# Performance work log

Hardware: AMD Instinct MI355X
Metric: run time of the kernel (lower is better)

## Reference

```python
import jax, jax.numpy as jnp
import numpy as np

B, C, H, W = 8, 128, 64, 64
D_STATE = 16
D_CONV = 4
EXPAND = 1.25
D_INNER = int(EXPAND * C)        # 160
DT_RANK = int(np.ceil(C / 16))   # 8


def setup_inputs() -> dict:
    key = jax.random.key(0)
    ks = jax.random.split(key, 10)
    f = lambda k, s, sc=0.02: jax.random.normal(k, s, dtype=jnp.float32) * sc
    return {
        "x": jax.random.normal(ks[0], (B, C, H, W), dtype=jnp.float32),
        "ln_g": jnp.ones((C,), jnp.float32),
        "ln_b": jnp.zeros((C,), jnp.float32),
        "in_proj_w": f(ks[1], (2 * D_INNER, C)),
        "conv_w": f(ks[2], (D_INNER, 1, D_CONV)),            # depthwise causal conv kernel
        "conv_b": jnp.zeros((D_INNER,), jnp.float32),
        "x_proj_w": f(ks[3], (DT_RANK + 2 * D_STATE, D_INNER)),
        "dt_proj_w": f(ks[4], (D_INNER, DT_RANK), 0.1),
        "dt_proj_b": f(ks[5], (D_INNER,), 0.1),
        # S4-style init: A_log = log(1..d_state) per inner channel (frozen in torch module)
        "A_log": jnp.log(jnp.tile(jnp.arange(1, D_STATE + 1, dtype=jnp.float32), (D_INNER, 1))),
        "D_param": jnp.ones((D_INNER,), jnp.float32),
        "out_proj_w": f(ks[6], (C, D_INNER)),
        "fuse_w": f(ks[7], (C, 2 * C)),                      # 1x1 conv == per-token matmul
        "scale": jnp.ones((1,), jnp.float32) * 0.1,
    }


def _layernorm(x, g, b, eps=1e-5):
    m = x.mean(-1, keepdims=True)
    v = x.var(-1, keepdims=True)
    return (x - m) * jax.lax.rsqrt(v + eps) * g + b


def _mamba(seq, in_proj_w, conv_w, conv_b, x_proj_w, dt_proj_w, dt_proj_b,
           A_log, D_param, out_proj_w):
    # seq: (B, L, C)
    Bsz, L, _ = seq.shape
    xz = jnp.einsum('blc,ec->ble', seq, in_proj_w)           # (B, L, 2*d_inner)
    xm, z = jnp.split(xz, 2, axis=-1)
    # depthwise causal conv over L, truncated to L (padding = d_conv-1 on the left)
    xc = jax.lax.conv_general_dilated(
        xm.transpose(0, 2, 1), conv_w, (1,), [(D_CONV - 1, 0)],
        feature_group_count=D_INNER, dimension_numbers=('NCH', 'OIH', 'NCH'))
    xm = jax.nn.silu((xc + conv_b[None, :, None]).transpose(0, 2, 1))  # (B, L, d_inner)
    x_dbl = jnp.einsum('bld,ed->ble', xm, x_proj_w)
    dt = x_dbl[..., :DT_RANK]
    Bm = x_dbl[..., DT_RANK:DT_RANK + D_STATE]               # (B, L, d_state)
    Cm = x_dbl[..., DT_RANK + D_STATE:]                      # (B, L, d_state)
    dt = jax.nn.softplus(jnp.einsum('blr,dr->bld', dt, dt_proj_w) + dt_proj_b)
    A = -jnp.exp(A_log)                                      # (d_inner, d_state)

    def step(h, inp):
        dt_t, B_t, C_t, x_t = inp                            # (B,d) (B,n) (B,n) (B,d)
        dA = jnp.exp(dt_t[:, :, None] * A)                   # (B, d_inner, d_state)
        h = dA * h + (dt_t * x_t)[:, :, None] * B_t[:, None, :]
        y = jnp.einsum('bdn,bn->bd', h, C_t)
        return h, y

    h0 = jnp.zeros((Bsz, D_INNER, D_STATE), dtype=seq.dtype)
    xs = (dt.transpose(1, 0, 2), Bm.transpose(1, 0, 2),
          Cm.transpose(1, 0, 2), xm.transpose(1, 0, 2))
    _, ys = jax.lax.scan(step, h0, xs)                       # ys: (L, B, d_inner)
    y = ys.transpose(1, 0, 2) + xm * D_param
    y = y * jax.nn.silu(z)
    return jnp.einsum('bld,cd->blc', y, out_proj_w)          # (B, L, C)


def reference(x, ln_g, ln_b, in_proj_w, conv_w, conv_b, x_proj_w, dt_proj_w,
              dt_proj_b, A_log, D_param, out_proj_w, fuse_w, scale):
    Bsz, Ch, Hh, Ww = x.shape
    seq = x.reshape(Bsz, Ch, Hh * Ww).transpose(0, 2, 1)     # (B, L, C) raster order
    seq_n = _layernorm(seq, ln_g, ln_b)                      # LN is per-token: commutes with flip
    args = (in_proj_w, conv_w, conv_b, x_proj_w, dt_proj_w, dt_proj_b,
            A_log, D_param, out_proj_w)
    y0 = _mamba(seq_n, *args)                                # forward raster scan
    y1 = _mamba(seq_n[:, ::-1, :], *args)[:, ::-1, :]        # reversed raster scan
    fused = jnp.einsum('blk,ck->blc', jnp.concatenate([y0, y1], axis=-1), fuse_w)
    out = seq + scale * fused                                # residual + learned scale
    return out.transpose(0, 2, 1).reshape(Bsz, Ch, Hh, Ww)
```

## Files before the change

### kernel.cpp

```cpp
#include <hip/hip_runtime.h>
#include <math.h>

#define LSEQ   4096
#define BATCH  8
#define CDIM   128
#define DIN    160
#define DSTATE 16
#define DTRANK 8
#define BLROWS (BATCH*LSEQ)
#define NCHUNK 128
#define TCH    32
#define SUBC   8
#define NSEG   16

typedef __attribute__((ext_vector_type(8))) short short8;
typedef __attribute__((ext_vector_type(8))) __bf16 bf16x8;
typedef __attribute__((ext_vector_type(4))) float float4v;
typedef __attribute__((ext_vector_type(2))) float f32x2;
typedef __attribute__((ext_vector_type(2))) unsigned u32x2;

__device__ __forceinline__ float4v mfma_bf16(short8 a, short8 b, float4v c) {
  return __builtin_amdgcn_mfma_f32_16x16x32_bf16(
      __builtin_bit_cast(bf16x8, a), __builtin_bit_cast(bf16x8, b), c, 0, 0, 0);
}

__device__ __forceinline__ unsigned short f2bf(float f) {
  union { float f; unsigned u; } v; v.f = f;
  unsigned r = v.u + 0x7FFF + ((v.u >> 16) & 1);
  return (unsigned short)(r >> 16);
}
__device__ __forceinline__ float bf2f(unsigned short h) {
  union { unsigned u; float f; } v; v.u = ((unsigned)h) << 16;
  return v.f;
}
__device__ __forceinline__ float f16tof(unsigned short h) {
  return (float)__builtin_bit_cast(_Float16, h);
}
__device__ __forceinline__ unsigned short ftof16(float f) {
  return __builtin_bit_cast(unsigned short, (_Float16)f);
}
__device__ __forceinline__ f32x2 pkfma(f32x2 a, f32x2 b, f32x2 c) {
#if __has_builtin(__builtin_elementwise_fma)
  return __builtin_elementwise_fma(a, b, c);
#else
  return a * b + c;
#endif
}
#define LO2(v) __builtin_shufflevector(v, v, 0, 1)
#define HI2(v) __builtin_shufflevector(v, v, 2, 3)

__global__ void prep_weights(const float* __restrict__ inpw, const float* __restrict__ xpw,
                             const float* __restrict__ fuse_w, const float* __restrict__ out_proj_w,
                             unsigned short* __restrict__ inpw_bf, unsigned short* __restrict__ xpw_bf,
                             unsigned short* __restrict__ W01) {
  int i = blockIdx.x * 256 + threadIdx.x;
  if (i < 320 * 128) inpw_bf[i] = f2bf(inpw[i]);
  if (i < 40 * 160)  xpw_bf[i]  = f2bf(xpw[i]);
  if (i < CDIM * DIN) {
    int d = i % DIN, c = i / DIN;
    float a0 = 0.f, a1 = 0.f;
    for (int k = 0; k < CDIM; ++k) {
      float o = out_proj_w[k * DIN + d];
      a0 += fuse_w[c * 256 + k] * o;
      a1 += fuse_w[c * 256 + 128 + k] * o;
    }
    W01[c * DIN + d] = f2bf(a0);
    W01[CDIM * DIN + c * DIN + d] = f2bf(a1);
  }
}

__global__ void ln_transpose_kernel(const float* __restrict__ x,
                                    const float* __restrict__ g,
                                    const float* __restrict__ bb,
                                    unsigned short* __restrict__ seqn) {
  __shared__ float sA[128 * 65];
  __shared__ float psum[2 * 256];
  __shared__ float mrs[2 * 64];
  int l0 = blockIdx.x * 64;
  int b  = blockIdx.y;
  int t  = threadIdx.x;
  int lsub = t & 63, crow = t >> 6;
  const float* xb = x + (size_t)b * CDIM * LSEQ;
  for (int it = 0; it < 32; ++it) {
    int c = crow + it * 4;
    sA[c * 65 + lsub] = xb[(size_t)c * LSEQ + l0 + lsub];
  }
  __syncthreads();
  float s = 0.f, ss = 0.f;
  for (int j = 0; j < 32; ++j) {
    int c = crow * 32 + j;
    float v = sA[c * 65 + lsub];
    s += v; ss += v * v;
  }
  psum[crow * 64 + lsub] = s;
  psum[256 + crow * 64 + lsub] = ss;
  __syncthreads();
  if (t < 64) {
    float su = 0.f, sq = 0.f;
    for (int p = 0; p < 4; ++p) { su += psum[p * 64 + t]; sq += psum[256 + p * 64 + t]; }
    float m = su * (1.f / 128.f);
    float var = sq * (1.f / 128.f) - m * m;
    mrs[t] = m;
    mrs[64 + t] = rsqrtf(var + 1e-5f);
  }
  __syncthreads();
  int c = t & 127, half = t >> 7;
  float gc = g[c], bc = bb[c];
  for (int it = 0; it < 32; ++it) {
    int l = it * 2 + half;
    float v = (sA[c * 65 + l] - mrs[l]) * mrs[64 + l] * gc + bc;
    seqn[((size_t)(b * LSEQ + l0 + l)) * CDIM + c] = f2bf(v);
  }
}

template<int K, bool MASKN, bool BF16OUT>
__global__ __launch_bounds__(256)
void gemm_mfma(const unsigned short* __restrict__ A0, const unsigned short* __restrict__ A1,
               const unsigned short* __restrict__ W,
               void* __restrict__ C0, void* __restrict__ C1, int N) {
  constexpr int LSTR = K + 8;
  __shared__ __align__(16) unsigned short As[64 * LSTR];
  __shared__ __align__(16) unsigned short Ws[64 * LSTR];
  const unsigned short* A = blockIdx.z ? A1 : A0;
  void* Cp = blockIdx.z ? C1 : C0;
  int m0 = blockIdx.x * 64;
  int n0 = blockIdx.y * 64;
  int t = threadIdx.x;
  constexpr int CH = 64 * K / 8;
  for (int c = t; c < CH; c += 256) {
    int row = c / (K / 8);
    int col = (c % (K / 8)) * 8;
    *(short8*)&As[row * LSTR + col] = *(const short8*)&A[(size_t)(m0 + row) * K + col];
    short8 wv = {};
    int nr = n0 + row;
    if (!MASKN || nr < N) wv = *(const short8*)&W[(size_t)nr * K + col];
    *(short8*)&Ws[row * LSTR + col] = wv;
  }
  __syncthreads();
  int lane = t & 63;
  int w = t >> 6;
  int l15 = lane & 15, quad = lane >> 4;
  float4v acc[4] = {};
#pragma unroll
  for (int kk = 0; kk < K; kk += 32) {
    short8 bfrag = *(const short8*)&Ws[(w * 16 + l15) * LSTR + kk + quad * 8];
#pragma unroll
    for (int i = 0; i < 4; ++i) {
      short8 afrag = *(const short8*)&As[(i * 16 + l15) * LSTR + kk + quad * 8];
      acc[i] = mfma_bf16(afrag, bfrag, acc[i]);
    }
  }
  int col = n0 + w * 16 + l15;
  if (MASKN && col >= N) return;
#pragma unroll
  for (int i = 0; i < 4; ++i)
#pragma unroll
    for (int r = 0; r < 4; ++r) {
      int row = m0 + i * 16 + quad * 4 + r;
      if (BF16OUT) ((unsigned short*)Cp)[(size_t)row * N + col] = f2bf(acc[i][r]);
      else         ((float*)Cp)[(size_t)row * N + col] = acc[i][r];
    }
}

__global__ void conv_silu_kernel(const unsigned short* __restrict__ xz,
                                 const float* __restrict__ cw,
                                 const float* __restrict__ cb,
                                 unsigned short* __restrict__ xm0,
                                 unsigned short* __restrict__ xm1,
                                 _Float16* __restrict__ szp) {
  int idx = blockIdx.x * 256 + threadIdx.x;
  int dir = blockIdx.y;
  if (idx >= BLROWS * 80) return;
  int dp = idx % 80;
  int bl = idx / 80;
  int l = bl % LSEQ, b = bl / LSEQ;
  int d = dp * 2;
  float w0[4], w1[4];
#pragma unroll
  for (int k = 0; k < 4; ++k) { w0[k] = cw[d * 4 + k]; w1[k] = cw[d * 4 + 4 + k]; }
  float a0 = cb[d], a1 = cb[d + 1];
  const unsigned short* base = xz + ((size_t)b * LSEQ) * 320 + d;
  if (dir == 0) {
#pragma unroll
    for (int k = 0; k < 4; ++k) {
      int lp = l - 3 + k;
      if (lp >= 0) {
        unsigned v = *(const unsigned*)&base[(size_t)lp * 320];
        a0 += w0[k] * bf2f((unsigned short)v);
        a1 += w1[k] * bf2f((unsigned short)(v >> 16));
      }
    }
  } else {
#pragma unroll
    for (int k = 0; k < 4; ++k) {
      int lp = l + 3 - k;
      if (lp < LSEQ) {
        unsigned v = *(const unsigned*)&base[(size_t)lp * 320];
        a0 += w0[k] * bf2f((unsigned short)v);
        a1 += w1[k] * bf2f((unsigned short)(v >> 16));
      }
    }
  }
  float s0 = a0 * __builtin_amdgcn_rcpf(1.f + __expf(-a0));
  float s1 = a1 * __builtin_amdgcn_rcpf(1.f + __expf(-a1));
  unsigned outv = (unsigned)f2bf(s0) | ((unsigned)f2bf(s1) << 16);
  unsigned short* xm = dir ? xm1 : xm0;
  *(unsigned*)&xm[(size_t)bl * DIN + d] = outv;
  if (dir == 0) {
    unsigned zv = *(const unsigned*)&xz[(size_t)bl * 320 + 160 + d];
    float z0 = bf2f((unsigned short)zv), z1 = bf2f((unsigned short)(zv >> 16));
    float g0 = z0 * __builtin_amdgcn_rcpf(1.f + __expf(-z0));
    float g1 = z1 * __builtin_amdgcn_rcpf(1.f + __expf(-z1));
    *(unsigned*)&szp[(size_t)bl * DIN + d] = (unsigned)ftof16(g0) | ((unsigned)ftof16(g1) << 16);
  }
}

__global__ void dtprep(const float* __restrict__ xdbl0, const float* __restrict__ xdbl1,
                       const float* __restrict__ dtw, const float* __restrict__ dtb,
                       unsigned* __restrict__ UR0, unsigned* __restrict__ UR1) {
  int idx = blockIdx.x * 256 + threadIdx.x;
  int dir = blockIdx.y;
  if (idx >= BLROWS * 80) return;
  int dp = idx % 80;
  int bl = idx / 80;
  const float* xdbl = dir ? xdbl1 : xdbl0;
  unsigned* UR = dir ? UR1 : UR0;
  float xr[8];
#pragma unroll
  for (int r = 0; r < 8; ++r) xr[r] = xdbl[(size_t)bl * 40 + r];
  unsigned out[2];
#pragma unroll
  for (int q = 0; q < 2; ++q) {
    int d = dp * 2 + q;
    float zz = dtb[d];
#pragma unroll
    for (int r = 0; r < 8; ++r) zz += xr[r] * dtw[d * 8 + r];
    float e  = __expf(fminf(zz, 20.f));
    float dt = (zz > 20.f) ? zz : __logf(1.f + e);
    float r1 = __builtin_amdgcn_rcpf(1.f + e);
    out[q] = (unsigned)ftof16(dt) | ((unsigned)ftof16(r1) << 16);
  }
  u32x2 o2 = { out[0], out[1] };
  *(u32x2*)&UR[(size_t)bl * DIN + dp * 2] = o2;
}

__global__ __launch_bounds__(320)
void scan_passA(const float* __restrict__ xdbl0, const float* __restrict__ xdbl1,
                const unsigned* __restrict__ UR0, const unsigned* __restrict__ UR1,
                const unsigned short* __restrict__ xm0v, const unsigned short* __restrict__ xm1v,
                const float* __restrict__ Dp,
                float* __restrict__ Q, float* __restrict__ rcf,
                unsigned* __restrict__ yr0, unsigned* __restrict__ yr1) {
  __shared__ __align__(16) float sBC[TCH * 32];
  int chunk = blockIdx.x, b = blockIdx.y, dir = blockIdx.z;
  int t = threadIdx.x;
  const float* xdbl = dir ? xdbl1 : xdbl0;
  const unsigned* UR = dir ? UR1 : UR0;
  const unsigned short* xm = dir ? xm1v : xm0v;
  unsigned* yr = dir ? yr1 : yr0;
  int l00 = dir ? (LSEQ - 1 - chunk * TCH) : (chunk * TCH);
  int step = dir ? -1 : 1;
  int rowbase = b * LSEQ + l00;
  for (int i = t; i < TCH * 32; i += 320) {
    int tt = i >> 5, j = i & 31;
    sBC[i] = xdbl[(size_t)(rowbase + step * tt) * 40 + 8 + j];
  }
  __syncthreads();
  int d = t >> 1, half = t & 1;
  float Dd = Dp[d];
  f32x2 h2[4] = {};
  float rcum = 1.f;
  const unsigned* urp = UR + (size_t)rowbase * DIN + d;
  const unsigned short* xmp = xm + (size_t)rowbase * DIN + d;
  unsigned* yrp = yr + (size_t)rowbase * DIN + d;
  int sstep = step * DIN;
  unsigned urb[4]; unsigned short xmb[4];
#pragma unroll
  for (int j = 0; j < 4; ++j) { urb[j] = urp[sstep * j]; xmb[j] = xmp[sstep * j]; }
  for (int g = 0; g < TCH / 4; ++g) {
#pragma unroll
    for (int j = 0; j < 4; ++j) {
      int tt = g * 4 + j;
      unsigned urv = urb[j];
      float xmv = bf2f(xmb[j]);
      if (g < TCH / 4 - 1) {
        urb[j] = urp[sstep * (tt + 4)];
        xmb[j] = xmp[sstep * (tt + 4)];
      }
      float dtv = f16tof((unsigned short)(urv & 0xFFFF));
      float r1  = f16tof((unsigned short)(urv >> 16));
      float u = dtv * xmv;
      rcum *= r1;
      float r2 = r1 * r1, r4 = r2 * r2, r8 = r4 * r4;
      float bs = half ? r8 : 1.f;
      f32x2 r2v = { r2, r2 };
      f32x2 p0 = { r1, r2 };
      f32x2 p1 = p0 * r2v;
      f32x2 p2 = p1 * r2v;
      f32x2 p3 = p2 * r2v;
      f32x2 bsv = { bs, bs };
      p0 *= bsv; p1 *= bsv; p2 *= bsv; p3 *= bsv;
      const float* bp = &sBC[tt * 32 + half * 8];
      float4v B0 = *(const float4v*)bp;
      float4v B1 = *(const float4v*)(bp + 4);
      float4v C0 = *(const float4v*)(bp + 16);
      float4v C1 = *(const float4v*)(bp + 20);
      f32x2 uv = { u, u };
      h2[0] = pkfma(p0, h2[0], uv * LO2(B0));
      h2[1] = pkfma(p1, h2[1], uv * HI2(B0));
      h2[2] = pkfma(p2, h2[2], uv * LO2(B1));
      h2[3] = pkfma(p3, h2[3], uv * HI2(B1));
      f32x2 ya = h2[0] * LO2(C0);
      ya = pkfma(h2[1], HI2(C0), ya);
      f32x2 yb = h2[2] * LO2(C1);
      yb = pkfma(h2[3], HI2(C1), yb);
      ya += yb;
      float ysc = ya[0] + ya[1];
      float yo = ysc + __shfl_xor(ysc, 1);
      if (half == 0) {
        float y = yo + Dd * xmv;
        yrp[sstep * tt] = (unsigned)f2bf(y) | ((unsigned)ftof16(rcum) << 16);
      }
    }
  }
  size_t base = (size_t)((dir * BATCH + b) * NCHUNK + chunk);
  float4v* qp = (float4v*)&Q[base * (DIN * 16) + d * 16 + half * 8];
  float4v q0 = { h2[0][0], h2[0][1], h2[1][0], h2[1][1] };
  float4v q1 = { h2[2][0], h2[2][1], h2[3][0], h2[3][1] };
  qp[0] = q0; qp[1] = q1;
  if (half == 0) rcf[base * DIN + d] = rcum;
}

__global__ __launch_bounds__(256)
void scan_passB(const float* Q, const float* __restrict__ rcf,
                float* Hinit) {
  __shared__ float sA[NSEG * 16], sQ[NSEG * 16];
  int blk = blockIdx.x;
  int d = blk % DIN;
  int rem = blk / DIN;
  int t = threadIdx.x;
  int n = t & 15, cs = t >> 4;
  unsigned k = n + 1;
  float a[SUBC], q[SUBC];
  float Aseg = 1.f, Qseg = 0.f;
#pragma unroll
  for (int j = 0; j < SUBC; ++j) {
    int ch = cs * SUBC + j;
    size_t base = (size_t)rem * NCHUNK + ch;
    float rf = rcf[base * DIN + d];
    float r2 = rf * rf, r4 = r2 * r2, r8 = r4 * r4;
    float av = 1.f;
    if (k & 1) av *= rf;
    if (k & 2) av *= r2;
    if (k & 4) av *= r4;
    if (k & 8) av *= r8;
    if (k & 16) av = r8 * r8;
    float qv = Q[base * (DIN * 16) + d * 16 + n];
    a[j] = av; q[j] = qv;
    Qseg = av * Qseg + qv;
    Aseg *= av;
  }
  sA[cs * 16 + n] = Aseg;
  sQ[cs * 16 + n] = Qseg;
  __syncthreads();
  if (t < 16) {
    float h = 0.f;
    for (int s = 0; s < NSEG; ++s) {
      float Av = sA[s * 16 + t], Qv = sQ[s * 16 + t];
      sA[s * 16 + t] = h;
      h = Av * h + Qv;
    }
  }
  __syncthreads();
  float h = sA[cs * 16 + n];
#pragma unroll
  for (int j = 0; j < SUBC; ++j) {
    int ch = cs * SUBC + j;
    size_t base = (size_t)rem * NCHUNK + ch;
    Hinit[base * (DIN * 16) + d * 16 + n] = h;
    h = a[j] * h + q[j];
  }
}

__global__ __launch_bounds__(192)
void scan_passC(const float* __restrict__ xdbl0, const float* __restrict__ xdbl1,
                const _Float16* __restrict__ szp,
                const float* __restrict__ Hinit,
                const unsigned* __restrict__ yr0, const unsigned* __restrict__ yr1,
                unsigned short* __restrict__ yg0, unsigned short* __restrict__ yg1) {
  __shared__ __align__(16) float sC[TCH * 16];
  int chunk = blockIdx.x, b = blockIdx.y, dir = blockIdx.z;
  int t = threadIdx.x;
  const float* xdbl = dir ? xdbl1 : xdbl0;
  const unsigned* yrb0 = dir ? yr1 : yr0;
  unsigned short* yg = dir ? yg1 : yg0;
  int l00 = dir ? (LSEQ - 1 - chunk * TCH) : (chunk * TCH);
  int step = dir ? -1 : 1;
  int rowbase = b * LSEQ + l00;
  for (int i = t; i < TCH * 16; i += 192)
    sC[i] = xdbl[(size_t)(rowbase + step * (i >> 4)) * 40 + 24 + (i & 15)];
  __syncthreads();
  if (t >= DIN) return;
  int d = t;
  size_t base = (size_t)((dir * BATCH + b) * NCHUNK + chunk);
  float4v H0v[4];
  const float4v* hp = (const float4v*)&Hinit[base * (DIN * 16) + d * 16];
#pragma unroll
  for (int n = 0; n < 4; ++n) H0v[n] = hp[n];
  const unsigned* yrp = yrb0 + (size_t)rowbase * DIN + d;
  const unsigned short* szq = (const unsigned short*)szp + (size_t)rowbase * DIN + d;
  unsigned short* ygp = yg + (size_t)rowbase * DIN + d;
  int sstep = step * DIN;
  unsigned yb[8]; unsigned short sb[8];
#pragma unroll
  for (int j = 0; j < 8; ++j) { yb[j] = yrp[sstep * j]; sb[j] = szq[sstep * j]; }
  for (int g = 0; g < TCH / 8; ++g) {
#pragma unroll
    for (int j = 0; j < 8; ++j) {
      int tt = g * 8 + j;
      unsigned v = yb[j];
      float sz = f16tof(sb[j]);
      if (g < TCH / 8 - 1) {
        yb[j] = yrp[sstep * (tt + 8)];
        sb[j] = szq[sstep * (tt + 8)];
      }
      float y = bf2f((unsigned short)v);
      float r1 = f16tof((unsigned short)(v >> 16));
      const float* cr = &sC[tt * 16];
      float4v Cv0 = *(const float4v*)cr;
      float4v Cv1 = *(const float4v*)(cr + 4);
      float4v Cv2 = *(const float4v*)(cr + 8);
      float4v Cv3 = *(const float4v*)(cr + 12);
      float r2 = r1 * r1;
      f32x2 r2v = { r2, r2 };
      f32x2 p0 = { r1, r2 };
      f32x2 p1 = p0 * r2v;
      f32x2 p2 = p1 * r2v;
      f32x2 p3 = p2 * r2v;
      f32x2 p4 = p3 * r2v;
      f32x2 p5 = p4 * r2v;
      f32x2 p6 = p5 * r2v;
      f32x2 p7 = p6 * r2v;
      f32x2 ca = p0 * (LO2(Cv0) * LO2(H0v[0]));
      ca = pkfma(p1, HI2(Cv0) * HI2(H0v[0]), ca);
      ca = pkfma(p2, LO2(Cv1) * LO2(H0v[1]), ca);
      ca = pkfma(p3, HI2(Cv1) * HI2(H0v[1]), ca);
      f32x2 cb2 = p4 * (LO2(Cv2) * LO2(H0v[2]));
      cb2 = pkfma(p5, HI2(Cv2) * HI2(H0v[2]), cb2);
      cb2 = pkfma(p6, LO2(Cv3) * LO2(H0v[3]), cb2);
      cb2 = pkfma(p7, HI2(Cv3) * HI2(H0v[3]), cb2);
      ca += cb2;
      float corr = ca[0] + ca[1];
      ygp[sstep * tt] = f2bf((y + corr) * sz);
    }
  }
}

__global__ __launch_bounds__(256)
void final_mfma(const unsigned short* __restrict__ yg0, const unsigned short* __restrict__ yg1,
                const unsigned short* __restrict__ W01, const float* __restrict__ x,
                const float* __restrict__ scale, float* __restrict__ out) {
  constexpr int K = DIN, LSTR = K + 8;
  __shared__ __align__(16) unsigned short As[64 * LSTR];
  __shared__ __align__(16) unsigned short Ws[64 * LSTR];
  float* sC = (float*)As;
  int m0 = blockIdx.x * 64;
  int c0 = blockIdx.y * 64;
  int b = m0 / LSEQ, l0 = m0 % LSEQ;
  int t = threadIdx.x;
  int lane = t & 63;
  int w = t >> 6;
  int l15 = lane & 15, quad = lane >> 4;
  float4v acc[4] = {};
  for (int pass = 0; pass < 2; ++pass) {
    const unsigned short* A = pass ? yg1 : yg0;
    const unsigned short* W = W01 + pass * (CDIM * K);
    if (pass) __syncthreads();
    constexpr int CH = 64 * K / 8;
    for (int c = t; c < CH; c += 256) {
      int row = c / (K / 8);
      int col = (c % (K / 8)) * 8;
      *(short8*)&As[row * LSTR + col] = *(const short8*)&A[(size_t)(m0 + row) * K + col];
      *(short8*)&Ws[row * LSTR + col] = *(const short8*)&W[(size_t)(c0 + row) * K + col];
    }
    __syncthreads();
#pragma unroll
    for (int kk = 0; kk < K; kk += 32) {
      short8 bfrag = *(const short8*)&Ws[(w * 16 + l15) * LSTR + kk + quad * 8];
#pragma unroll
      for (int i = 0; i < 4; ++i) {
        short8 afrag = *(const short8*)&As[(i * 16 + l15) * LSTR + kk + quad * 8];
        acc[i] = mfma_bf16(afrag, bfrag, acc[i]);
      }
    }
  }
  __syncthreads();
#pragma unroll
  for (int i = 0; i < 4; ++i)
#pragma unroll
    for (int r = 0; r < 4; ++r)
      sC[(i * 16 + quad * 4 + r) * 65 + w * 16 + l15] = acc[i][r];
  __syncthreads();
  float sc = scale[0];
  int ll = t & 63, cq = t >> 6;
#pragma unroll
  for (int j = 0; j < 16; ++j) {
    int cl = cq * 16 + j;
    float v = sC[ll * 65 + cl];
    size_t gi = ((size_t)(b * CDIM + c0 + cl)) * LSEQ + l0 + ll;
    out[gi] = x[gi] + sc * v;
  }
}

extern "C" void kernel_launch(void* const* d_in, const int* in_sizes, int n_in,
                              void* d_out, int out_size, void* d_ws, size_t ws_size,
                              hipStream_t stream) {
  const float* x        = (const float*)d_in[0];
  const float* ln_g     = (const float*)d_in[1];
  const float* ln_b     = (const float*)d_in[2];
  const float* in_projw = (const float*)d_in[3];
  const float* conv_w   = (const float*)d_in[4];
  const float* conv_b   = (const float*)d_in[5];
  const float* x_projw  = (const float*)d_in[6];
  const float* dt_projw = (const float*)d_in[7];
  const float* dt_projb = (const float*)d_in[8];
  const float* A_log    = (const float*)d_in[9];
  const float* D_param  = (const float*)d_in[10];
  const float* out_projw= (const float*)d_in[11];
  const float* fuse_w   = (const float*)d_in[12];
  const float* scale    = (const float*)d_in[13];
  float* out = (float*)d_out;
  (void)A_log;

  float* ws = (float*)d_ws;
  size_t off = 0;
  unsigned short* seqn_bf = (unsigned short*)(ws + off); off += (size_t)BLROWS * CDIM / 2;
  unsigned short* xz      = (unsigned short*)(ws + off); off += (size_t)BLROWS * 320 / 2;
  unsigned* UR0 = (unsigned*)xz;
  unsigned short* xm0 = (unsigned short*)(ws + off); off += (size_t)BLROWS * DIN / 2;
  unsigned short* xm1 = (unsigned short*)(ws + off); off += (size_t)BLROWS * DIN / 2;
  float* xdbl0 = ws + off; off += (size_t)BLROWS * 40;
  float* xdbl1 = ws + off; off += (size_t)BLROWS * 40;
  float* Q     = ws + off; off += (size_t)2 * BATCH * NCHUNK * DIN * 16;
  float* Hinit = Q;
  float* rcf   = ws + off; off += (size_t)2 * BATCH * NCHUNK * DIN;
  unsigned* yr0 = (unsigned*)(ws + off); off += (size_t)BLROWS * DIN;
  unsigned* yr1 = (unsigned*)(ws + off); off += (size_t)BLROWS * DIN;
  unsigned short* yg0 = (unsigned short*)(ws + off); off += (size_t)BLROWS * DIN / 2;
  unsigned short* yg1 = (unsigned short*)(ws + off); off += (size_t)BLROWS * DIN / 2;
  _Float16* szv = (_Float16*)(ws + off); off += (size_t)BLROWS * DIN / 2;
  unsigned* UR1 = (unsigned*)(ws + off); off += (size_t)BLROWS * DIN;
  unsigned short* W01bf = (unsigned short*)(ws + off); off += (size_t)2 * CDIM * DIN / 2;
  unsigned short* inpw_bf = (unsigned short*)(ws + off); off += (size_t)320 * 128 / 2;
  unsigned short* xpw_bf  = (unsigned short*)(ws + off); off += (size_t)40 * 160 / 2 + 8;

  prep_weights<<<(320 * 128 + 255) / 256, 256, 0, stream>>>(
      in_projw, x_projw, fuse_w, out_projw, inpw_bf, xpw_bf, W01bf);
  ln_transpose_kernel<<<dim3(LSEQ / 64, BATCH), 256, 0, stream>>>(x, ln_g, ln_b, seqn_bf);
  gemm_mfma<128, false, true><<<dim3(BLROWS / 64, 5, 1), 256, 0, stream>>>(
      seqn_bf, seqn_bf, inpw_bf, xz, xz, 320);
  conv_silu_kernel<<<dim3((BLROWS * 80 + 255) / 256, 2), 256, 0, stream>>>(
      xz, conv_w, conv_b, xm0, xm1, szv);
  gemm_mfma<160, true, false><<<dim3(BLROWS / 64, 1, 2), 256, 0, stream>>>(
      xm0, xm1, xpw_bf, xdbl0, xdbl1, 40);
  dtprep<<<dim3((BLROWS * 80 + 255) / 256, 2), 256, 0, stream>>>(
      xdbl0, xdbl1, dt_projw, dt_projb, UR0, UR1);
  scan_passA<<<dim3(NCHUNK, BATCH, 2), 320, 0, stream>>>(xdbl0, xdbl1, UR0, UR1, xm0, xm1,
                                                         D_param, Q, rcf, yr0, yr1);
  scan_passB<<<2 * BATCH * DIN, 256, 0, stream>>>(Q, rcf, Hinit);
  scan_passC<<<dim3(NCHUNK, BATCH, 2), 192, 0, stream>>>(xdbl0, xdbl1, szv, Hinit,
                                                         yr0, yr1, yg0, yg1);
  final_mfma<<<dim3(BLROWS / 64, CDIM / 64), 256, 0, stream>>>(yg0, yg1, W01bf, x, scale, out);
}
```

Baseline: 267.4 us.

## Fuse dt projection into scan passes and recompute chunk scan in pass C

After: 287.0 us. 1.07x slower.

```diff
diff --git a/kernel.cpp b/kernel.cpp
--- a/kernel.cpp
+++ b/kernel.cpp
@@ -17,7 +17,6 @@
 typedef __attribute__((ext_vector_type(8))) __bf16 bf16x8;
 typedef __attribute__((ext_vector_type(4))) float float4v;
 typedef __attribute__((ext_vector_type(2))) float f32x2;
-typedef __attribute__((ext_vector_type(2))) unsigned u32x2;
 
 __device__ __forceinline__ float4v mfma_bf16(short8 a, short8 b, float4v c) {
   return __builtin_amdgcn_mfma_f32_16x16x32_bf16(
@@ -215,113 +214,75 @@
   }
 }
 
-__global__ void dtprep(const float* __restrict__ xdbl0, const float* __restrict__ xdbl1,
-                       const float* __restrict__ dtw, const float* __restrict__ dtb,
-                       unsigned* __restrict__ UR0, unsigned* __restrict__ UR1) {
-  int idx = blockIdx.x * 256 + threadIdx.x;
-  int dir = blockIdx.y;
-  if (idx >= BLROWS * 80) return;
-  int dp = idx % 80;
-  int bl = idx / 80;
-  const float* xdbl = dir ? xdbl1 : xdbl0;
-  unsigned* UR = dir ? UR1 : UR0;
-  float xr[8];
-#pragma unroll
-  for (int r = 0; r < 8; ++r) xr[r] = xdbl[(size_t)bl * 40 + r];
-  unsigned out[2];
-#pragma unroll
-  for (int q = 0; q < 2; ++q) {
-    int d = dp * 2 + q;
-    float zz = dtb[d];
-#pragma unroll
-    for (int r = 0; r < 8; ++r) zz += xr[r] * dtw[d * 8 + r];
-    float e  = __expf(fminf(zz, 20.f));
-    float dt = (zz > 20.f) ? zz : __logf(1.f + e);
-    float r1 = __builtin_amdgcn_rcpf(1.f + e);
-    out[q] = (unsigned)ftof16(dt) | ((unsigned)ftof16(r1) << 16);
-  }
-  u32x2 o2 = { out[0], out[1] };
-  *(u32x2*)&UR[(size_t)bl * DIN + dp * 2] = o2;
-}
-
 __global__ __launch_bounds__(320)
 void scan_passA(const float* __restrict__ xdbl0, const float* __restrict__ xdbl1,
-                const unsigned* __restrict__ UR0, const unsigned* __restrict__ UR1,
                 const unsigned short* __restrict__ xm0v, const unsigned short* __restrict__ xm1v,
-                const float* __restrict__ Dp,
-                float* __restrict__ Q, float* __restrict__ rcf,
-                unsigned* __restrict__ yr0, unsigned* __restrict__ yr1) {
-  __shared__ __align__(16) float sBC[TCH * 32];
+                const float* __restrict__ dtw, const float* __restrict__ dtb,
+                float* __restrict__ Q, float* __restrict__ rcf) {
+  __shared__ __align__(16) float sX[TCH * 40];
+  __shared__ unsigned sUR[TCH * DIN];
+  __shared__ float sWt[8 * DIN];
+  __shared__ float sDB[DIN];
   int chunk = blockIdx.x, b = blockIdx.y, dir = blockIdx.z;
   int t = threadIdx.x;
   const float* xdbl = dir ? xdbl1 : xdbl0;
-  const unsigned* UR = dir ? UR1 : UR0;
   const unsigned short* xm = dir ? xm1v : xm0v;
-  unsigned* yr = dir ? yr1 : yr0;
   int l00 = dir ? (LSEQ - 1 - chunk * TCH) : (chunk * TCH);
   int step = dir ? -1 : 1;
   int rowbase = b * LSEQ + l00;
-  for (int i = t; i < TCH * 32; i += 320) {
-    int tt = i >> 5, j = i & 31;
-    sBC[i] = xdbl[(size_t)(rowbase + step * tt) * 40 + 8 + j];
+  for (int i = t; i < 8 * DIN; i += 320) {
+    int dd = i >> 3, r = i & 7;
+    sWt[r * DIN + dd] = dtw[i];
+  }
+  if (t < DIN) sDB[t] = dtb[t];
+  for (int i = t; i < TCH * 40; i += 320) {
+    int tt = i / 40, j = i - tt * 40;
+    sX[i] = xdbl[(size_t)(rowbase + step * tt) * 40 + j];
+  }
+  __syncthreads();
+  {
+    int dd = (t < DIN) ? t : (t - DIN);
+    int toff = (t < DIN) ? 0 : 1;
+    float db = sDB[dd];
+#pragma unroll
+    for (int k = 0; k < TCH / 2; ++k) {
+      int tt = k * 2 + toff;
+      float zz = db;
+#pragma unroll
+      for (int r = 0; r < 8; ++r) zz += sX[tt * 40 + r] * sWt[r * DIN + dd];
+      float e  = __expf(fminf(zz, 20.f));
+      float dt = (zz > 20.f) ? zz : __logf(1.f + e);
+      float r1 = __builtin_amdgcn_rcpf(1.f + e);
+      float xmv = bf2f(xm[(size_t)(rowbase + step * tt) * DIN + dd]);
+      float u = dt * xmv;
+      sUR[tt * DIN + dd] = (unsigned)ftof16(u) | ((unsigned)ftof16(r1) << 16);
+    }
   }
   __syncthreads();
   int d = t >> 1, half = t & 1;
-  float Dd = Dp[d];
   f32x2 h2[4] = {};
   float rcum = 1.f;
-  const unsigned* urp = UR + (size_t)rowbase * DIN + d;
-  const unsigned short* xmp = xm + (size_t)rowbase * DIN + d;
-  unsigned* yrp = yr + (size_t)rowbase * DIN + d;
-  int sstep = step * DIN;
-  unsigned urb[4]; unsigned short xmb[4];
-#pragma unroll
-  for (int j = 0; j < 4; ++j) { urb[j] = urp[sstep * j]; xmb[j] = xmp[sstep * j]; }
-  for (int g = 0; g < TCH / 4; ++g) {
-#pragma unroll
-    for (int j = 0; j < 4; ++j) {
-      int tt = g * 4 + j;
-      unsigned urv = urb[j];
-      float xmv = bf2f(xmb[j]);
-      if (g < TCH / 4 - 1) {
-        urb[j] = urp[sstep * (tt + 4)];
-        xmb[j] = xmp[sstep * (tt + 4)];
-      }
-      float dtv = f16tof((unsigned short)(urv & 0xFFFF));
-      float r1  = f16tof((unsigned short)(urv >> 16));
-      float u = dtv * xmv;
-      rcum *= r1;
-      float r2 = r1 * r1, r4 = r2 * r2, r8 = r4 * r4;
-      float bs = half ? r8 : 1.f;
-      f32x2 r2v = { r2, r2 };
-      f32x2 p0 = { r1, r2 };
-      f32x2 p1 = p0 * r2v;
-      f32x2 p2 = p1 * r2v;
-      f32x2 p3 = p2 * r2v;
-      f32x2 bsv = { bs, bs };
-      p0 *= bsv; p1 *= bsv; p2 *= bsv; p3 *= bsv;
-      const float* bp = &sBC[tt * 32 + half * 8];
-      float4v B0 = *(const float4v*)bp;
-      float4v B1 = *(const float4v*)(bp + 4);
-      float4v C0 = *(const float4v*)(bp + 16);
-      float4v C1 = *(const float4v*)(bp + 20);
-      f32x2 uv = { u, u };
-      h2[0] = pkfma(p0, h2[0], uv * LO2(B0));
-      h2[1] = pkfma(p1, h2[1], uv * HI2(B0));
-      h2[2] = pkfma(p2, h2[2], uv * LO2(B1));
-      h2[3] = pkfma(p3, h2[3], uv * HI2(B1));
-      f32x2 ya = h2[0] * LO2(C0);
-      ya = pkfma(h2[1], HI2(C0), ya);
-      f32x2 yb = h2[2] * LO2(C1);
-      yb = pkfma(h2[3], HI2(C1), yb);
-      ya += yb;
-      float ysc = ya[0] + ya[1];
-      float yo = ysc + __shfl_xor(ysc, 1);
-      if (half == 0) {
-        float y = yo + Dd * xmv;
-        yrp[sstep * tt] = (unsigned)f2bf(y) | ((unsigned)ftof16(rcum) << 16);
-      }
-    }
+#pragma unroll 4
+  for (int tt = 0; tt < TCH; ++tt) {
+    unsigned urv = sUR[tt * DIN + d];
+    float u  = f16tof((unsigned short)(urv & 0xFFFF));
+    float r1 = f16tof((unsigned short)(urv >> 16));
+    rcum *= r1;
+    float r2 = r1 * r1, r4 = r2 * r2, r8 = r4 * r4;
+    float bs = half ? r8 : 1.f;
+    f32x2 r2v = { r2, r2 };
+    f32x2 p0 = { r1, r2 };
+    f32x2 p1 = p0 * r2v, p2 = p1 * r2v, p3 = p2 * r2v;
+    f32x2 bsv = { bs, bs };
+    p0 *= bsv; p1 *= bsv; p2 *= bsv; p3 *= bsv;
+    const float* bp = &sX[tt * 40 + 8 + half * 8];
+    float4v B0 = *(const float4v*)bp;
+    float4v B1 = *(const float4v*)(bp + 4);
+    f32x2 uv = { u, u };
+    h2[0] = pkfma(p0, h2[0], uv * LO2(B0));
+    h2[1] = pkfma(p1, h2[1], uv * HI2(B0));
+    h2[2] = pkfma(p2, h2[2], uv * LO2(B1));
+    h2[3] = pkfma(p3, h2[3], uv * HI2(B1));
   }
   size_t base = (size_t)((dir * BATCH + b) * NCHUNK + chunk);
   float4v* qp = (float4v*)&Q[base * (DIN * 16) + d * 16 + half * 8];
@@ -382,76 +343,105 @@
   }
 }
 
-__global__ __launch_bounds__(192)
+__global__ __launch_bounds__(320)
 void scan_passC(const float* __restrict__ xdbl0, const float* __restrict__ xdbl1,
-                const _Float16* __restrict__ szp,
+                const unsigned short* __restrict__ xm0v, const unsigned short* __restrict__ xm1v,
+                const _Float16* __restrict__ szp, const float* __restrict__ Dp,
+                const float* __restrict__ dtw, const float* __restrict__ dtb,
                 const float* __restrict__ Hinit,
-                const unsigned* __restrict__ yr0, const unsigned* __restrict__ yr1,
                 unsigned short* __restrict__ yg0, unsigned short* __restrict__ yg1) {
-  __shared__ __align__(16) float sC[TCH * 16];
+  __shared__ __align__(16) float sX[TCH * 40];
+  __shared__ unsigned sUR[TCH * DIN];
+  __shared__ unsigned sYS[TCH * DIN];
+  __shared__ float sWt[8 * DIN];
+  __shared__ float sDB[DIN];
+  __shared__ float sD[DIN];
   int chunk = blockIdx.x, b = blockIdx.y, dir = blockIdx.z;
   int t = threadIdx.x;
   const float* xdbl = dir ? xdbl1 : xdbl0;
-  const unsigned* yrb0 = dir ? yr1 : yr0;
+  const unsigned short* xm = dir ? xm1v : xm0v;
+  const unsigned short* szq = (const unsigned short*)szp;
   unsigned short* yg = dir ? yg1 : yg0;
   int l00 = dir ? (LSEQ - 1 - chunk * TCH) : (chunk * TCH);
   int step = dir ? -1 : 1;
   int rowbase = b * LSEQ + l00;
-  for (int i = t; i < TCH * 16; i += 192)
-    sC[i] = xdbl[(size_t)(rowbase + step * (i >> 4)) * 40 + 24 + (i & 15)];
-  __syncthreads();
-  if (t >= DIN) return;
-  int d = t;
+  for (int i = t; i < 8 * DIN; i += 320) {
+    int dd = i >> 3, r = i & 7;
+    sWt[r * DIN + dd] = dtw[i];
+  }
+  if (t < DIN) { sDB[t] = dtb[t]; sD[t] = Dp[t]; }
+  for (int i = t; i < TCH * 40; i += 320) {
+    int tt = i / 40, j = i - tt * 40;
+    sX[i] = xdbl[(size_t)(rowbase + step * tt) * 40 + j];
+  }
+  __syncthreads();
+  {
+    int dd = (t < DIN) ? t : (t - DIN);
+    int toff = (t < DIN) ? 0 : 1;
+    float db = sDB[dd];
+    float Dd = sD[dd];
+#pragma unroll
+    for (int k = 0; k < TCH / 2; ++k) {
+      int tt = k * 2 + toff;
+      float zz = db;
+#pragma unroll
+      for (int r = 0; r < 8; ++r) zz += sX[tt * 40 + r] * sWt[r * DIN + dd];
+      float e  = __expf(fminf(zz, 20.f));
+      float dt = (zz > 20.f) ? zz : __logf(1.f + e);
+      float r1 = __builtin_amdgcn_rcpf(1.f + e);
+      size_t gi = (size_t)(rowbase + step * tt) * DIN + dd;
+      float xmv = bf2f(xm[gi]);
+      float u = dt * xmv;
+      sUR[tt * DIN + dd] = (unsigned)ftof16(u) | ((unsigned)ftof16(r1) << 16);
+      float szf = f16tof(szq[gi]);
+      float ofs = Dd * xmv * szf;
+      sYS[tt * DIN + dd] = (unsigned)ftof16(szf) | ((unsigned)ftof16(ofs) << 16);
+    }
+  }
+  __syncthreads();
+  int d = t >> 1, half = t & 1;
   size_t base = (size_t)((dir * BATCH + b) * NCHUNK + chunk);
-  float4v H0v[4];
-  const float4v* hp = (const float4v*)&Hinit[base * (DIN * 16) + d * 16];
-#pragma unroll
-  for (int n = 0; n < 4; ++n) H0v[n] = hp[n];
-  const unsigned* yrp = yrb0 + (size_t)rowbase * DIN + d;
-  const unsigned short* szq = (const unsigned short*)szp + (size_t)rowbase * DIN + d;
+  const float4v* hp = (const float4v*)&Hinit[base * (DIN * 16) + d * 16 + half * 8];
+  float4v H0a = hp[0], H0b = hp[1];
+  f32x2 h2[4] = { {H0a[0], H0a[1]}, {H0a[2], H0a[3]},
+                  {H0b[0], H0b[1]}, {H0b[2], H0b[3]} };
   unsigned short* ygp = yg + (size_t)rowbase * DIN + d;
   int sstep = step * DIN;
-  unsigned yb[8]; unsigned short sb[8];
-#pragma unroll
-  for (int j = 0; j < 8; ++j) { yb[j] = yrp[sstep * j]; sb[j] = szq[sstep * j]; }
-  for (int g = 0; g < TCH / 8; ++g) {
-#pragma unroll
-    for (int j = 0; j < 8; ++j) {
-      int tt = g * 8 + j;
-      unsigned v = yb[j];
-      float sz = f16tof(sb[j]);
-      if (g < TCH / 8 - 1) {
-        yb[j] = yrp[sstep * (tt + 8)];
-        sb[j] = szq[sstep * (tt + 8)];
-      }
-      float y = bf2f((unsigned short)v);
-      float r1 = f16tof((unsigned short)(v >> 16));
-      const float* cr = &sC[tt * 16];
-      float4v Cv0 = *(const float4v*)cr;
-      float4v Cv1 = *(const float4v*)(cr + 4);
-      float4v Cv2 = *(const float4v*)(cr + 8);
-      float4v Cv3 = *(const float4v*)(cr + 12);
-      float r2 = r1 * r1;
-      f32x2 r2v = { r2, r2 };
-      f32x2 p0 = { r1, r2 };
-      f32x2 p1 = p0 * r2v;
-      f32x2 p2 = p1 * r2v;
-      f32x2 p3 = p2 * r2v;
-      f32x2 p4 = p3 * r2v;
-      f32x2 p5 = p4 * r2v;
-      f32x2 p6 = p5 * r2v;
-      f32x2 p7 = p6 * r2v;
-      f32x2 ca = p0 * (LO2(Cv0) * LO2(H0v[0]));
-      ca = pkfma(p1, HI2(Cv0) * HI2(H0v[0]), ca);
-      ca = pkfma(p2, LO2(Cv1) * LO2(H0v[1]), ca);
-      ca = pkfma(p3, HI2(Cv1) * HI2(H0v[1]), ca);
-      f32x2 cb2 = p4 * (LO2(Cv2) * LO2(H0v[2]));
-      cb2 = pkfma(p5, HI2(Cv2) * HI2(H0v[2]), cb2);
-      cb2 = pkfma(p6, LO2(Cv3) * LO2(H0v[3]), cb2);
-      cb2 = pkfma(p7, HI2(Cv3) * HI2(H0v[3]), cb2);
-      ca += cb2;
-      float corr = ca[0] + ca[1];
-      ygp[sstep * tt] = f2bf((y + corr) * sz);
+#pragma unroll 4
+  for (int tt = 0; tt < TCH; ++tt) {
+    unsigned urv = sUR[tt * DIN + d];
+    float u  = f16tof((unsigned short)(urv & 0xFFFF));
+    float r1 = f16tof((unsigned short)(urv >> 16));
+    float r2 = r1 * r1, r4 = r2 * r2, r8 = r4 * r4;
+    float bs = half ? r8 : 1.f;
+    f32x2 r2v = { r2, r2 };
+    f32x2 p0 = { r1, r2 };
+    f32x2 p1 = p0 * r2v, p2 = p1 * r2v, p3 = p2 * r2v;
+    f32x2 bsv = { bs, bs };
+    p0 *= bsv; p1 *= bsv; p2 *= bsv; p3 *= bsv;
+    const float* bp = &sX[tt * 40 + 8 + half * 8];
+    float4v B0 = *(const float4v*)bp;
+    float4v B1 = *(const float4v*)(bp + 4);
+    f32x2 uv = { u, u };
+    h2[0] = pkfma(p0, h2[0], uv * LO2(B0));
+    h2[1] = pkfma(p1, h2[1], uv * HI2(B0));
+    h2[2] = pkfma(p2, h2[2], uv * LO2(B1));
+    h2[3] = pkfma(p3, h2[3], uv * HI2(B1));
+    const float* cp = &sX[tt * 40 + 24 + half * 8];
+    float4v C0 = *(const float4v*)cp;
+    float4v C1 = *(const float4v*)(cp + 4);
+    f32x2 ya = h2[0] * LO2(C0);
+    ya = pkfma(h2[1], HI2(C0), ya);
+    f32x2 yb = h2[2] * LO2(C1);
+    yb = pkfma(h2[3], HI2(C1), yb);
+    ya += yb;
+    float ysc = ya[0] + ya[1];
+    float yo = ysc + __shfl_xor(ysc, 1);
+    if (half == 0) {
+      unsigned ysv = sYS[tt * DIN + d];
+      float szf = f16tof((unsigned short)(ysv & 0xFFFF));
+      float ofs = f16tof((unsigned short)(ysv >> 16));
+      ygp[sstep * tt] = f2bf(yo * szf + ofs);
     }
   }
 }
@@ -536,7 +526,6 @@
   size_t off = 0;
   unsigned short* seqn_bf = (unsigned short*)(ws + off); off += (size_t)BLROWS * CDIM / 2;
   unsigned short* xz      = (unsigned short*)(ws + off); off += (size_t)BLROWS * 320 / 2;
-  unsigned* UR0 = (unsigned*)xz;
   unsigned short* xm0 = (unsigned short*)(ws + off); off += (size_t)BLROWS * DIN / 2;
   unsigned short* xm1 = (unsigned short*)(ws + off); off += (size_t)BLROWS * DIN / 2;
   float* xdbl0 = ws + off; off += (size_t)BLROWS * 40;
@@ -544,12 +533,9 @@
   float* Q     = ws + off; off += (size_t)2 * BATCH * NCHUNK * DIN * 16;
   float* Hinit = Q;
   float* rcf   = ws + off; off += (size_t)2 * BATCH * NCHUNK * DIN;
-  unsigned* yr0 = (unsigned*)(ws + off); off += (size_t)BLROWS * DIN;
-  unsigned* yr1 = (unsigned*)(ws + off); off += (size_t)BLROWS * DIN;
   unsigned short* yg0 = (unsigned short*)(ws + off); off += (size_t)BLROWS * DIN / 2;
   unsigned short* yg1 = (unsigned short*)(ws + off); off += (size_t)BLROWS * DIN / 2;
   _Float16* szv = (_Float16*)(ws + off); off += (size_t)BLROWS * DIN / 2;
-  unsigned* UR1 = (unsigned*)(ws + off); off += (size_t)BLROWS * DIN;
   unsigned short* W01bf = (unsigned short*)(ws + off); off += (size_t)2 * CDIM * DIN / 2;
   unsigned short* inpw_bf = (unsigned short*)(ws + off); off += (size_t)320 * 128 / 2;
   unsigned short* xpw_bf  = (unsigned short*)(ws + off); off += (size_t)40 * 160 / 2 + 8;
@@ -563,12 +549,11 @@
       xz, conv_w, conv_b, xm0, xm1, szv);
   gemm_mfma<160, true, false><<<dim3(BLROWS / 64, 1, 2), 256, 0, stream>>>(
       xm0, xm1, xpw_bf, xdbl0, xdbl1, 40);
-  dtprep<<<dim3((BLROWS * 80 + 255) / 256, 2), 256, 0, stream>>>(
-      xdbl0, xdbl1, dt_projw, dt_projb, UR0, UR1);
-  scan_passA<<<dim3(NCHUNK, BATCH, 2), 320, 0, stream>>>(xdbl0, xdbl1, UR0, UR1, xm0, xm1,
-                                                         D_param, Q, rcf, yr0, yr1);
+  scan_passA<<<dim3(NCHUNK, BATCH, 2), 320, 0, stream>>>(xdbl0, xdbl1, xm0, xm1,
+                                                         dt_projw, dt_projb, Q, rcf);
   scan_passB<<<2 * BATCH * DIN, 256, 0, stream>>>(Q, rcf, Hinit);
-  scan_passC<<<dim3(NCHUNK, BATCH, 2), 192, 0, stream>>>(xdbl0, xdbl1, szv, Hinit,
-                                                         yr0, yr1, yg0, yg1);
+  scan_passC<<<dim3(NCHUNK, BATCH, 2), 320, 0, stream>>>(xdbl0, xdbl1, xm0, xm1,
+                                                         szv, D_param, dt_projw, dt_projb,
+                                                         Hinit, yg0, yg1);
   final_mfma<<<dim3(BLROWS / 64, CDIM / 64), 256, 0, stream>>>(yg0, yg1, W01bf, x, scale, out);
 }
```
